# Optimization experiments

Hardware: AMD Instinct MI355X
Metric: run time of the kernel (lower is better)

The kernel has to match this reference:

```python
import jax, jax.numpy as jnp
import numpy as np

EXPERT_NUM = 8
SEQ_LEN = 2048
FREQ_LEN = SEQ_LEN // 2 + 1
B, C = 32, 512


def setup_inputs() -> dict:
    key = jax.random.key(0)
    k1, k2, k3 = jax.random.split(key, 3)
    x = jax.random.normal(k1, (B, C, SEQ_LEN), dtype=jnp.float32)
    band_boundaries = jax.random.uniform(k2, (EXPERT_NUM - 1,), dtype=jnp.float32)
    gate_w = jax.random.normal(k3, (EXPERT_NUM, FREQ_LEN), dtype=jnp.float32) / np.sqrt(FREQ_LEN)
    gate_b = jnp.zeros((EXPERT_NUM,), dtype=jnp.float32)
    return {"x": x, "band_boundaries": band_boundaries, "gate_w": gate_w, "gate_b": gate_b}


def reference(x, band_boundaries, gate_w, gate_b):
    # x: [B, C, L].  Normalize across channels per (batch, time) position.
    xp = jnp.transpose(x, (0, 2, 1))                       # [B, L, C]
    x_mean = jnp.mean(xp, axis=2, keepdims=True)           # [B, L, 1]
    xc = xp - x_mean
    x_var = jnp.var(xc, axis=2, keepdims=True, ddof=1) + 1e-5  # unbiased, as torch.var
    xn = xc / jnp.sqrt(x_var)
    x_norm = jnp.transpose(xn, (0, 2, 1))                  # [B, C, L]

    freq_x = jnp.fft.rfft(x_norm, axis=-1)                 # [B, C, F] complex
    F = FREQ_LEN

    # Learnable band boundaries -> integer bin boundaries per expert.
    b = jnp.sort(jax.nn.sigmoid(band_boundaries))
    b = jnp.concatenate([jnp.zeros((1,), b.dtype), b, jnp.ones((1,), b.dtype)])
    idx = (b * F).astype(jnp.int32)
    idx = idx.at[-1].set(F)                                # [E+1]

    # Per-frequency-bin expert membership: [E, F] 0/1 mask.
    f = jnp.arange(F)
    member = ((f[None, :] >= idx[:-1, None]) & (f[None, :] < idx[1:, None])).astype(x.dtype)

    # Gating over mean spectral magnitude.
    gating_input = jnp.abs(freq_x).mean(axis=1)            # [B, F]
    gating_scores = jax.nn.softmax(gating_input @ gate_w.T + gate_b, axis=-1)  # [B, E]

    # Fused: per-bin gate weight = sum_e g[b,e] * member[e,f] (no E copies of freq_x).
    w = gating_scores @ member                             # [B, F]
    combined_freq = freq_x * w[:, None, :].astype(freq_x.dtype)

    combined = jnp.fft.irfft(combined_freq, n=SEQ_LEN, axis=-1)  # [B, C, L]

    # De-normalize.
    cp = jnp.transpose(combined, (0, 2, 1))                # [B, L, C]
    out = cp * jnp.sqrt(x_var) + x_mean
    return jnp.transpose(out, (0, 2, 1))                   # [B, C, L]
```

## Files before the change

kernel.cpp:

```cpp
#include <hip/hip_runtime.h>
#include <math.h>

#define NB 32
#define NC 512
#define NF 1025

#define WS_MEAN 0
#define WS_SSTD 65536
#define WS_RSTD 131072
#define WS_GACC 196608
#define WS_WGT  229408
#define WS_PART 262208
#define WS_END_SPLIT (262208 + 262144)
#define WS_SPEC WS_END_SPLIT
#define WS_SPEC_FLOATS (NB * NC * 2048)
#define WS_END_CACHE (WS_SPEC + WS_SPEC_FLOATS)
#define WS_GPART WS_END_CACHE
#define WS_GPART_FLOATS (NB * 64 * NF)
#define WS_END_GPART (WS_GPART + WS_GPART_FLOATS)

#define PIDX(a) ((a) + ((a) >> 4))

__device__ __forceinline__ void lds_barrier() {
  __builtin_amdgcn_sched_barrier(0);
  asm volatile("s_waitcnt lgkmcnt(0)" ::: "memory");
  __builtin_amdgcn_s_barrier();
  __builtin_amdgcn_sched_barrier(0);
}

__device__ __forceinline__ void stage4_body(const float* __restrict__ sr,
                                            const float* __restrict__ si,
                                            float* __restrict__ dr,
                                            float* __restrict__ di,
                                            const int ls, const float w1c, const float w1s,
                                            const bool fwd) {
  const int t = threadIdx.x;
  const int s = 1 << ls;
  const int q = t & (s - 1);
  const int p = t >> ls;
  const float ar = sr[PIDX(t)],       ai = si[PIDX(t)];
  const float br = sr[PIDX(t + 256)], bi = si[PIDX(t + 256)];
  const float cr = sr[PIDX(t + 512)], ci = si[PIDX(t + 512)];
  const float er = sr[PIDX(t + 768)], ei = si[PIDX(t + 768)];
  const float apcr = ar + cr, apci = ai + ci;
  const float amcr = ar - cr, amci = ai - ci;
  const float bpdr = br + er, bpdi = bi + ei;
  const float bmdr = br - er, bmdi = bi - ei;
  const float w2r = w1c * w1c - w1s * w1s, w2i = 2.0f * w1c * w1s;
  const float w3r = w2r * w1c - w2i * w1s, w3i = w2r * w1s + w2i * w1c;
  float u1r, u1i, u3r, u3i;
  if (fwd) {
    u1r = amcr + bmdi; u1i = amci - bmdr;
    u3r = amcr - bmdi; u3i = amci + bmdr;
  } else {
    u1r = amcr - bmdi; u1i = amci + bmdr;
    u3r = amcr + bmdi; u3i = amci - bmdr;
  }
  const float x0r = apcr + bpdr, x0i = apci + bpdi;
  const float v2r = apcr - bpdr, v2i = apci - bpdi;
  const float x1r = w1c * u1r - w1s * u1i, x1i = w1c * u1i + w1s * u1r;
  const float x2r = w2r * v2r - w2i * v2i, x2i = w2r * v2i + w2i * v2r;
  const float x3r = w3r * u3r - w3i * u3i, x3i = w3r * u3i + w3i * u3r;
  const int base = q + ((p << 2) << ls);
  dr[PIDX(base)] = x0r;             di[PIDX(base)] = x0i;
  dr[PIDX(base + s)] = x1r;         di[PIDX(base + s)] = x1i;
  dr[PIDX(base + 2 * s)] = x2r;     di[PIDX(base + 2 * s)] = x2i;
  dr[PIDX(base + 3 * s)] = x3r;     di[PIDX(base + 3 * s)] = x3i;
}

__device__ __forceinline__ void stage4(const float* __restrict__ sr,
                                       const float* __restrict__ si,
                                       float* __restrict__ dr,
                                       float* __restrict__ di,
                                       const int ls, const float w1c, const float w1s,
                                       const bool fwd) {
  lds_barrier();
  stage4_body(sr, si, dr, di, ls, w1c, w1s, fwd);
}

__device__ __forceinline__ void stage0_reg(const float2 z0, const float2 z1,
                                           const float2 z2, const float2 z3,
                                           float* __restrict__ dr, float* __restrict__ di,
                                           const float w1c, const float w1s,
                                           const bool fwd) {
  const int t = threadIdx.x;
  const float apcr = z0.x + z2.x, apci = z0.y + z2.y;
  const float amcr = z0.x - z2.x, amci = z0.y - z2.y;
  const float bpdr = z1.x + z3.x, bpdi = z1.y + z3.y;
  const float bmdr = z1.x - z3.x, bmdi = z1.y - z3.y;
  const float w2r = w1c * w1c - w1s * w1s, w2i = 2.0f * w1c * w1s;
  const float w3r = w2r * w1c - w2i * w1s, w3i = w2r * w1s + w2i * w1c;
  float u1r, u1i, u3r, u3i;
  if (fwd) {
    u1r = amcr + bmdi; u1i = amci - bmdr;
    u3r = amcr - bmdi; u3i = amci + bmdr;
  } else {
    u1r = amcr - bmdi; u1i = amci + bmdr;
    u3r = amcr + bmdi; u3i = amci - bmdr;
  }
  const float x0r = apcr + bpdr, x0i = apci + bpdi;
  const float v2r = apcr - bpdr, v2i = apci - bpdi;
  const float x1r = w1c * u1r - w1s * u1i, x1i = w1c * u1i + w1s * u1r;
  const float x2r = w2r * v2r - w2i * v2i, x2i = w2r * v2i + w2i * v2r;
  const float x3r = w3r * u3r - w3i * u3i, x3i = w3r * u3i + w3i * u3r;
  const int base = t << 2;
  dr[PIDX(base)] = x0r;         di[PIDX(base)] = x0i;
  dr[PIDX(base + 1)] = x1r;     di[PIDX(base + 1)] = x1i;
  dr[PIDX(base + 2)] = x2r;     di[PIDX(base + 2)] = x2i;
  dr[PIDX(base + 3)] = x3r;     di[PIDX(base + 3)] = x3i;
}

__device__ __forceinline__ void stage_nt_body(const float* __restrict__ sr,
                                              const float* __restrict__ si,
                                              float2& o0, float2& o1, float2& o2, float2& o3,
                                              const bool fwd) {
  const int t = threadIdx.x;
  const float ar = sr[PIDX(t)],       ai = si[PIDX(t)];
  const float br = sr[PIDX(t + 256)], bi = si[PIDX(t + 256)];
  const float cr = sr[PIDX(t + 512)], ci = si[PIDX(t + 512)];
  const float er = sr[PIDX(t + 768)], ei = si[PIDX(t + 768)];
  const float apcr = ar + cr, apci = ai + ci;
  const float amcr = ar - cr, amci = ai - ci;
  const float bpdr = br + er, bpdi = bi + ei;
  const float bmdr = br - er, bmdi = bi - ei;
  float u1r, u1i, u3r, u3i;
  if (fwd) {
    u1r = amcr + bmdi; u1i = amci - bmdr;
    u3r = amcr - bmdi; u3i = amci + bmdr;
  } else {
    u1r = amcr - bmdi; u1i = amci + bmdr;
    u3r = amcr + bmdi; u3i = amci - bmdr;
  }
  o0.x = apcr + bpdr;  o0.y = apci + bpdi;
  o1.x = u1r;          o1.y = u1i;
  o2.x = apcr - bpdr;  o2.y = apci - bpdi;
  o3.x = u3r;          o3.y = u3i;
}

__device__ __forceinline__ void stage_nt_reg(const float* __restrict__ sr,
                                             const float* __restrict__ si,
                                             float2& o0, float2& o1, float2& o2, float2& o3,
                                             const bool fwd) {
  lds_barrier();
  stage_nt_body(sr, si, o0, o1, o2, o3, fwd);
}

__device__ __forceinline__ void fft_twiddles(int t, float& c0, float& s0,
                                             float& c1, float& s1,
                                             float& c2, float& s2,
                                             float& c3, float& s3) {
  __sincosf(-0.00613592315f * (float)t, &s0, &c0);
  __sincosf(-0.02454369261f * (float)(t >> 2), &s1, &c1);
  __sincosf(-0.09817477042f * (float)(t >> 4), &s2, &c2);
  __sincosf(-0.39269908170f * (float)(t >> 6), &s3, &c3);
}

__global__ __launch_bounds__(256) void kmoments(const float* __restrict__ x,
                                                float* __restrict__ ws) {
  const int b = blockIdx.x >> 3;
  const int l = ((blockIdx.x & 7) << 8) + threadIdx.x;
  const float* px = x + (size_t)b * (NC * 2048) + l;
  float sum = 0.f, sq = 0.f;
#pragma unroll 16
  for (int c = 0; c < NC; ++c) {
    float v = px[(size_t)c * 2048];
    sum += v;
    sq = fmaf(v, v, sq);
  }
  float mean = sum * (1.0f / 512.0f);
  float var = fmaf(-512.0f * mean, mean, sq) * (1.0f / 511.0f) + 1e-5f;
  float ss = sqrtf(var);
  int o = (b << 11) + l;
  ws[WS_MEAN + o] = mean;
  ws[WS_SSTD + o] = ss;
  ws[WS_RSTD + o] = 1.0f / ss;
}

__global__ __launch_bounds__(256) void kmoments_part(const float* __restrict__ x,
                                                     float* __restrict__ ws) {
  const int b = blockIdx.x >> 3;
  const int l = ((blockIdx.x & 7) << 8) + threadIdx.x;
  const int half = blockIdx.y;
  const float* px = x + (size_t)b * (NC * 2048) + (size_t)(half * 256) * 2048 + l;
  float sum = 0.f, sq = 0.f;
#pragma unroll 16
  for (int c = 0; c < 256; ++c) {
    float v = px[(size_t)c * 2048];
    sum += v;
    sq = fmaf(v, v, sq);
  }
  int o = (b << 11) + l;
  float2* part = (float2*)(ws + WS_PART) + (half << 16) + o;
  float2 pv; pv.x = sum; pv.y = sq;
  *part = pv;
}

__global__ __launch_bounds__(256) void kmoments_fin(float* __restrict__ ws) {
  const int o = blockIdx.x * 256 + threadIdx.x;
  const float2* part = (const float2*)(ws + WS_PART);
  float2 p0 = part[o];
  float2 p1 = part[(1 << 16) + o];
  float sum = p0.x + p1.x, sq = p0.y + p1.y;
  float mean = sum * (1.0f / 512.0f);
  float var = fmaf(-512.0f * mean, mean, sq) * (1.0f / 511.0f) + 1e-5f;
  float ss = sqrtf(var);
  ws[WS_MEAN + o] = mean;
  ws[WS_SSTD + o] = ss;
  ws[WS_RSTD + o] = 1.0f / ss;
}

__global__ __launch_bounds__(256) void kspec(const float* __restrict__ x,
                                             float* __restrict__ ws,
                                             float2* __restrict__ zout,
                                             float* __restrict__ gpart) {
  __shared__ float Ar[1088], Ai[1088], Br[1088], Bi[1088];
  const int tid = threadIdx.x;
  const int b = blockIdx.x >> 6;
  const int c0 = (blockIdx.x & 63) << 3;
  const float2* mean2 = (const float2*)(ws + WS_MEAN) + ((size_t)b << 10);
  const float2* rstd2 = (const float2*)(ws + WS_RSTD) + ((size_t)b << 10);
  float2 mv[4], rv[4];
#pragma unroll
  for (int j = 0; j < 4; ++j) {
    mv[j] = mean2[tid + (j << 8)];
    rv[j] = rstd2[tid + (j << 8)];
  }
  float w1s, w1c, w2s, w2c;
  __sincosf(-0.00306796158f * (float)tid, &w1s, &w1c);
  __sincosf(-0.00306796158f * (float)(tid + 256), &w2s, &w2c);
  float c0t, s0t, c1t, s1t, c2t, s2t, c3t, s3t;
  fft_twiddles(tid, c0t, s0t, c1t, s1t, c2t, s2t, c3t, s3t);
  float acc0 = 0.f, acc1 = 0.f, acc2 = 0.f, acc3 = 0.f, acc4 = 0.f;
  const float2* xrow = (const float2*)x + ((size_t)(b * NC + c0) << 10);
  float2 v[4];
#pragma unroll
  for (int j = 0; j < 4; ++j) v[j] = xrow[tid + (j << 8)];
  for (int r = 0; r < 8; ++r) {
    float2 zz[4];
#pragma unroll
    for (int j = 0; j < 4; ++j) {
      zz[j].x = (v[j].x - mv[j].x) * rv[j].x;
      zz[j].y = (v[j].y - mv[j].y) * rv[j].y;
    }
    if (r < 7) {
      const float2* nx = xrow + ((size_t)(r + 1) << 10);
#pragma unroll
      for (int j = 0; j < 4; ++j) v[j] = nx[tid + (j << 8)];
    }
    lds_barrier();
    stage0_reg(zz[0], zz[1], zz[2], zz[3], Br, Bi, c0t, s0t, true);
    stage4(Br, Bi, Ar, Ai, 2, c1t, s1t, true);
    stage4(Ar, Ai, Br, Bi, 4, c2t, s2t, true);
    stage4(Br, Bi, Ar, Ai, 6, c3t, s3t, true);
    float2 o0, o1, o2, o3;
    stage_nt_reg(Ar, Ai, o0, o1, o2, o3, true);
    Br[PIDX(tid)] = o0.x;        Bi[PIDX(tid)] = o0.y;
    Br[PIDX(tid + 256)] = o1.x;  Bi[PIDX(tid + 256)] = o1.y;
    Br[PIDX(tid + 512)] = o2.x;  Bi[PIDX(tid + 512)] = o2.y;
    Br[PIDX(tid + 768)] = o3.x;  Bi[PIDX(tid + 768)] = o3.y;
    lds_barrier();
    if (zout) {
      float2* zrow = zout + ((size_t)(b * NC + c0 + r) << 10);
      zrow[tid] = o0;
      zrow[tid + 256] = o1;
      zrow[tid + 512] = o2;
      zrow[tid + 768] = o3;
    }
    if (tid == 0) {
      float zr = Br[PIDX(0)], zi = Bi[PIDX(0)];
      acc0 += fabsf(zr + zi);
      acc1 += fabsf(zr - zi);
      float mr = Br[PIDX(512)], mi = Bi[PIDX(512)];
      acc4 += sqrtf(mr * mr + mi * mi);
    } else {
      const int k = tid;
      float zkr = Br[PIDX(k)], zki = Bi[PIDX(k)];
      float zmr = Br[PIDX(1024 - k)], zmi = Bi[PIDX(1024 - k)];
      float Ar_ = 0.5f * (zkr + zmr), Ai_ = 0.5f * (zki - zmi);
      float Br_ = 0.5f * (zki + zmi), Bi_ = -0.5f * (zkr - zmr);
      float WBr = Br_ * w1c - Bi_ * w1s, WBi = Br_ * w1s + Bi_ * w1c;
      float Xr = Ar_ + WBr, Xi = Ai_ + WBi;
      float Yr = Ar_ - WBr, Yi = Ai_ - WBi;
      acc0 += sqrtf(Xr * Xr + Xi * Xi);
      acc1 += sqrtf(Yr * Yr + Yi * Yi);
    }
    {
      const int k = tid + 256;
      float zkr = Br[PIDX(k)], zki = Bi[PIDX(k)];
      float zmr = Br[PIDX(1024 - k)], zmi = Bi[PIDX(1024 - k)];
      float Ar_ = 0.5f * (zkr + zmr), Ai_ = 0.5f * (zki - zmi);
      float Br_ = 0.5f * (zki + zmi), Bi_ = -0.5f * (zkr - zmr);
      float WBr = Br_ * w2c - Bi_ * w2s, WBi = Br_ * w2s + Bi_ * w2c;
      float Xr = Ar_ + WBr, Xi = Ai_ + WBi;
      float Yr = Ar_ - WBr, Yi = Ai_ - WBi;
      acc2 += sqrtf(Xr * Xr + Xi * Xi);
      acc3 += sqrtf(Yr * Yr + Yi * Yi);
    }
  }
  if (gpart) {
    float* prow = gpart + (size_t)blockIdx.x * NF;
    prow[tid] = acc0;
    prow[1024 - tid] = acc1;
    prow[tid + 256] = acc2;
    prow[768 - tid] = acc3;
    if (tid == 0) prow[512] = acc4;
  } else {
    float* g = ws + WS_GACC + b * NF;
    atomicAdd(g + tid, acc0);
    atomicAdd(g + 1024 - tid, acc1);
    atomicAdd(g + tid + 256, acc2);
    atomicAdd(g + 768 - tid, acc3);
    if (tid == 0) atomicAdd(g + 512, acc4);
  }
}

__global__ __launch_bounds__(256) void kgate(float* __restrict__ ws,
                                             const float* __restrict__ gw,
                                             const float* __restrict__ gb,
                                             const float* __restrict__ bb,
                                             const float* __restrict__ gpart) {
  const float* gacc = ws + WS_GACC;
  float* wgt = ws + WS_WGT;
  const int b = blockIdx.x;
  const int tid = threadIdx.x;
  __shared__ float red[256];
  __shared__ float sc[8];
  __shared__ int sidx[9];
  float acc[8];
#pragma unroll
  for (int e = 0; e < 8; ++e) acc[e] = 0.f;
  for (int f = tid; f < NF; f += 256) {
    float g;
    if (gpart) {
      const float* gp = gpart + (size_t)b * 64 * NF + f;
      g = 0.f;
#pragma unroll 8
      for (int j = 0; j < 64; ++j) g += gp[j * NF];
    } else {
      g = gacc[b * NF + f];
    }
    g *= (1.0f / 512.0f);
#pragma unroll
    for (int e = 0; e < 8; ++e) acc[e] = fmaf(g, gw[e * NF + f], acc[e]);
  }
#pragma unroll
  for (int e = 0; e < 8; ++e) {
    __syncthreads();
    red[tid] = acc[e];
    __syncthreads();
    for (int s2 = 128; s2 > 0; s2 >>= 1) {
      if (tid < s2) red[tid] += red[tid + s2];
      __syncthreads();
    }
    if (tid == 0) sc[e] = red[0] + gb[e];
  }
  __syncthreads();
  if (tid == 0) {
    float mx = sc[0];
    for (int e = 1; e < 8; ++e) mx = fmaxf(mx, sc[e]);
    float sum = 0.f;
    float ex[8];
    for (int e = 0; e < 8; ++e) { ex[e] = expf(sc[e] - mx); sum += ex[e]; }
    for (int e = 0; e < 8; ++e) sc[e] = ex[e] / sum;
    float sv[7];
    for (int i2 = 0; i2 < 7; ++i2) sv[i2] = 1.0f / (1.0f + expf(-bb[i2]));
    for (int i2 = 1; i2 < 7; ++i2) {
      float key = sv[i2];
      int j2 = i2 - 1;
      while (j2 >= 0 && sv[j2] > key) { sv[j2 + 1] = sv[j2]; --j2; }
      sv[j2 + 1] = key;
    }
    sidx[0] = 0;
    for (int i2 = 0; i2 < 7; ++i2) sidx[i2 + 1] = (int)(sv[i2] * 1025.0f);
    sidx[8] = 1025;
  }
  __syncthreads();
  for (int f = tid; f < NF; f += 256) {
    float wv = 0.f;
#pragma unroll
    for (int e = 0; e < 8; ++e)
      if (f >= sidx[e] && f < sidx[e + 1]) wv += sc[e];
    wgt[b * NF + f] = wv;
  }
}

__device__ __forceinline__ void combine_pair(float* __restrict__ zr_, float* __restrict__ zi_,
                                             int k, float wc, float ws_, float wk, float wmk) {
  const int ik = PIDX(k), im = PIDX(1024 - k);
  float zkr = zr_[ik], zki = zi_[ik];
  float zmr = zr_[im], zmi = zi_[im];
  float Ar_ = 0.5f * (zkr + zmr), Ai_ = 0.5f * (zki - zmi);
  float Br2 = 0.5f * (zki + zmi), Bi2 = -0.5f * (zkr - zmr);
  float WBr = Br2 * wc - Bi2 * ws_, WBi = Br2 * ws_ + Bi2 * wc;
  float Xr = Ar_ + WBr, Xi = Ai_ + WBi;
  float Xcr = Ar_ - WBr, Xci = Ai_ - WBi;
  float XpR = wk * Xr, XpI = wk * Xi;
  float XcpR = wmk * Xcr, XcpI = wmk * Xci;
  float Apr = 0.5f * (XpR + XcpR), Api = 0.5f * (XpI + XcpI);
  float Er = 0.5f * (XpR - XcpR), Ei = 0.5f * (XpI - XcpI);
  float Bpr = Er * wc + Ei * ws_;
  float Bpi = Ei * wc - Er * ws_;
  zr_[ik] = Apr - Bpi;  zi_[ik] = Api + Bpr;
  zr_[im] = Apr + Bpi;  zi_[im] = Bpr - Api;
}

__device__ __forceinline__ void combine_all(float* __restrict__ Br_, float* __restrict__ Bi_,
                                            const int tid,
                                            const float w1c, const float w1s,
                                            const float w2c, const float w2s,
                                            const float wk1, const float wm1,
                                            const float wk2, const float wm2,
                                            const float wmid) {
  if (tid == 0) {
    float zr = Br_[PIDX(0)], zi = Bi_[PIDX(0)];
    float X0 = (zr + zi) * wk1;
    float XM = (zr - zi) * wm1;
    Br_[PIDX(0)] = 0.5f * (X0 + XM);
    Bi_[PIDX(0)] = 0.5f * (X0 - XM);
    Br_[PIDX(512)] *= wmid;
    Bi_[PIDX(512)] *= wmid;
  } else {
    combine_pair(Br_, Bi_, tid, w1c, w1s, wk1, wm1);
  }
  combine_pair(Br_, Bi_, tid + 256, w2c, w2s, wk2, wm2);
}

__global__ __launch_bounds__(256) void kapply(const float* __restrict__ x,
                                              float* __restrict__ out,
                                              const float* __restrict__ ws) {
  __shared__ float Ar[1088], Ai[1088], Br[1088], Bi[1088];
  const int tid = threadIdx.x;
  const int b = blockIdx.x >> 9;
  const float2* mean2 = (const float2*)(ws + WS_MEAN) + ((size_t)b << 10);
  const float2* sstd2 = (const float2*)(ws + WS_SSTD) + ((size_t)b << 10);
  const float2* rstd2 = (const float2*)(ws + WS_RSTD) + ((size_t)b << 10);
  const float2* x2 = (const float2*)x + ((size_t)blockIdx.x << 10);
  const float* wrow = ws + WS_WGT + b * NF;
  float wk1 = wrow[tid];
  float wm1 = wrow[1024 - tid];
  float wk2 = wrow[tid + 256];
  float wm2 = wrow[768 - tid];
  float wmid = wrow[512];
  float w1s, w1c, w2s, w2c;
  __sincosf(-0.00306796158f * (float)tid, &w1s, &w1c);
  __sincosf(-0.00306796158f * (float)(tid + 256), &w2s, &w2c);
  float c0t, s0t, c1t, s1t, c2t, s2t, c3t, s3t;
  fft_twiddles(tid, c0t, s0t, c1t, s1t, c2t, s2t, c3t, s3t);
  float2 mv[4], rv[4], ssv[4];
#pragma unroll
  for (int j = 0; j < 4; ++j) {
    mv[j] = mean2[tid + (j << 8)];
    rv[j] = rstd2[tid + (j << 8)];
    ssv[j] = sstd2[tid + (j << 8)];
  }
  float2 zz[4];
#pragma unroll
  for (int j = 0; j < 4; ++j) {
    float2 v = x2[tid + (j << 8)];
    zz[j].x = (v.x - mv[j].x) * rv[j].x;
    zz[j].y = (v.y - mv[j].y) * rv[j].y;
  }
  stage0_reg(zz[0], zz[1], zz[2], zz[3], Br, Bi, c0t, s0t, true);
  stage4(Br, Bi, Ar, Ai, 2, c1t, s1t, true);
  stage4(Ar, Ai, Br, Bi, 4, c2t, s2t, true);
  stage4(Br, Bi, Ar, Ai, 6, c3t, s3t, true);
  float2 f0, f1, f2, f3;
  stage_nt_reg(Ar, Ai, f0, f1, f2, f3, true);
  Br[PIDX(tid)] = f0.x;        Bi[PIDX(tid)] = f0.y;
  Br[PIDX(tid + 256)] = f1.x;  Bi[PIDX(tid + 256)] = f1.y;
  Br[PIDX(tid + 512)] = f2.x;  Bi[PIDX(tid + 512)] = f2.y;
  Br[PIDX(tid + 768)] = f3.x;  Bi[PIDX(tid + 768)] = f3.y;
  lds_barrier();
  combine_all(Br, Bi, tid, w1c, w1s, w2c, w2s, wk1, wm1, wk2, wm2, wmid);
  stage4(Br, Bi, Ar, Ai, 0, c0t, -s0t, false);
  stage4(Ar, Ai, Br, Bi, 2, c1t, -s1t, false);
  stage4(Br, Bi, Ar, Ai, 4, c2t, -s2t, false);
  stage4(Ar, Ai, Br, Bi, 6, c3t, -s3t, false);
  float2 o0, o1, o2, o3;
  stage_nt_reg(Br, Bi, o0, o1, o2, o3, false);
  const float inv = 1.0f / 1024.0f;
  float2* out2 = (float2*)out + ((size_t)blockIdx.x << 10);
  float2 oo;
  oo.x = fmaf(o0.x * inv, ssv[0].x, mv[0].x);
  oo.y = fmaf(o0.y * inv, ssv[0].y, mv[0].y);
  out2[tid] = oo;
  oo.x = fmaf(o1.x * inv, ssv[1].x, mv[1].x);
  oo.y = fmaf(o1.y * inv, ssv[1].y, mv[1].y);
  out2[tid + 256] = oo;
  oo.x = fmaf(o2.x * inv, ssv[2].x, mv[2].x);
  oo.y = fmaf(o2.y * inv, ssv[2].y, mv[2].y);
  out2[tid + 512] = oo;
  oo.x = fmaf(o3.x * inv, ssv[3].x, mv[3].x);
  oo.y = fmaf(o3.y * inv, ssv[3].y, mv[3].y);
  out2[tid + 768] = oo;
}

__global__ __launch_bounds__(256) void kapply_z(const float2* __restrict__ z,
                                                float* __restrict__ out,
                                                const float* __restrict__ ws) {
  __shared__ float Ar[1088], Ai[1088], Br[1088], Bi[1088];
  const int tid = threadIdx.x;
  const int b = blockIdx.x >> 9;
  const float2* mean2 = (const float2*)(ws + WS_MEAN) + ((size_t)b << 10);
  const float2* sstd2 = (const float2*)(ws + WS_SSTD) + ((size_t)b << 10);
  const float* wrow = ws + WS_WGT + b * NF;
  float wk1 = wrow[tid];
  float wm1 = wrow[1024 - tid];
  float wk2 = wrow[tid + 256];
  float wm2 = wrow[768 - tid];
  float wmid = wrow[512];
  float w1s, w1c, w2s, w2c;
  __sincosf(-0.00306796158f * (float)tid, &w1s, &w1c);
  __sincosf(-0.00306796158f * (float)(tid + 256), &w2s, &w2c);
  float c0t, s0t, c1t, s1t, c2t, s2t, c3t, s3t;
  fft_twiddles(tid, c0t, s0t, c1t, s1t, c2t, s2t, c3t, s3t);
  const float2* zrow = z + ((size_t)blockIdx.x << 10);
  float2 mv[4], ssv[4];
#pragma unroll
  for (int j = 0; j < 4; ++j) {
    mv[j] = mean2[tid + (j << 8)];
    ssv[j] = sstd2[tid + (j << 8)];
  }
#pragma unroll
  for (int j = 0; j < 4; ++j) {
    const int n = tid + (j << 8);
    float2 v = zrow[n];
    Br[PIDX(n)] = v.x;
    Bi[PIDX(n)] = v.y;
  }
  lds_barrier();
  combine_all(Br, Bi, tid, w1c, w1s, w2c, w2s, wk1, wm1, wk2, wm2, wmid);
  stage4(Br, Bi, Ar, Ai, 0, c0t, -s0t, false);
  stage4(Ar, Ai, Br, Bi, 2, c1t, -s1t, false);
  stage4(Br, Bi, Ar, Ai, 4, c2t, -s2t, false);
  stage4(Ar, Ai, Br, Bi, 6, c3t, -s3t, false);
  float2 o0, o1, o2, o3;
  stage_nt_reg(Br, Bi, o0, o1, o2, o3, false);
  const float inv = 1.0f / 1024.0f;
  float2* out2 = (float2*)out + ((size_t)blockIdx.x << 10);
  float2 oo;
  oo.x = fmaf(o0.x * inv, ssv[0].x, mv[0].x);
  oo.y = fmaf(o0.y * inv, ssv[0].y, mv[0].y);
  out2[tid] = oo;
  oo.x = fmaf(o1.x * inv, ssv[1].x, mv[1].x);
  oo.y = fmaf(o1.y * inv, ssv[1].y, mv[1].y);
  out2[tid + 256] = oo;
  oo.x = fmaf(o2.x * inv, ssv[2].x, mv[2].x);
  oo.y = fmaf(o2.y * inv, ssv[2].y, mv[2].y);
  out2[tid + 512] = oo;
  oo.x = fmaf(o3.x * inv, ssv[3].x, mv[3].x);
  oo.y = fmaf(o3.y * inv, ssv[3].y, mv[3].y);
  out2[tid + 768] = oo;
}

extern "C" void kernel_launch(void* const* d_in, const int* in_sizes, int n_in,
                              void* d_out, int out_size, void* d_ws, size_t ws_size,
                              hipStream_t stream) {
  const float* x = (const float*)d_in[0];
  const float* bb = (const float*)d_in[1];
  const float* gw = (const float*)d_in[2];
  const float* gb = (const float*)d_in[3];
  float* ws = (float*)d_ws;
  float* out = (float*)d_out;

  const bool split = ws_size >= (size_t)WS_END_SPLIT * sizeof(float);
  const bool cache = ws_size >= (size_t)WS_END_CACHE * sizeof(float);
  const bool part = ws_size >= (size_t)WS_END_GPART * sizeof(float);

  if (!part) {
    hipMemsetAsync((char*)d_ws + WS_GACC * sizeof(float), 0, (NB * NF) * sizeof(float), stream);
  }
  if (split) {
    kmoments_part<<<dim3(NB * 8, 2), dim3(256), 0, stream>>>(x, ws);
    kmoments_fin<<<dim3(256), dim3(256), 0, stream>>>(ws);
  } else {
    kmoments<<<dim3(NB * 8), dim3(256), 0, stream>>>(x, ws);
  }
  kspec<<<dim3(NB * 64), dim3(256), 0, stream>>>(x, ws,
      cache ? (float2*)(ws + WS_SPEC) : nullptr,
      part ? (ws + WS_GPART) : nullptr);
  kgate<<<dim3(NB), dim3(256), 0, stream>>>(ws, gw, gb, bb,
      part ? (ws + WS_GPART) : nullptr);
  if (cache) {
    kapply_z<<<dim3(NB * NC), dim3(256), 0, stream>>>((const float2*)(ws + WS_SPEC), out, ws);
  } else {
    kapply<<<dim3(NB * NC), dim3(256), 0, stream>>>(x, out, ws);
  }
}
```

Before: 352.2 us.

## Interleave FFT shared buffers as float2 and precompute twiddle powers

Changes the LDS FFT scratch from separate real and imaginary float arrays to interleaved float2 arrays with a new padding scheme. Each element then moves in one 64-bit LDS access instead of two 32-bit ones, and stage0 writes use float4. Twiddle squares and cubes are now computed once per kernel rather than in every stage. The gating kernel also stops writing a full per-bin weight row. It stores only the expert scores and band indices, and the apply kernels rebuild per-bin weights in registers, which adds some ALU work and register pressure.

```diff
diff --git a/kernel.cpp b/kernel.cpp
--- a/kernel.cpp
+++ b/kernel.cpp
@@ -19,7 +19,7 @@
 #define WS_GPART_FLOATS (NB * 64 * NF)
 #define WS_END_GPART (WS_GPART + WS_GPART_FLOATS)
 
-#define PIDX(a) ((a) + ((a) >> 4))
+#define P2(a) ((a) + 2 * ((a) >> 4))
 
 __device__ __forceinline__ void lds_barrier() {
   __builtin_amdgcn_sched_barrier(0);
@@ -28,26 +28,31 @@
   __builtin_amdgcn_sched_barrier(0);
 }
 
-__device__ __forceinline__ void stage4_body(const float* __restrict__ sr,
-                                            const float* __restrict__ si,
-                                            float* __restrict__ dr,
-                                            float* __restrict__ di,
-                                            const int ls, const float w1c, const float w1s,
-                                            const bool fwd) {
+struct Tw { float c1, s1, c2, s2, c3, s3; };
+__device__ __forceinline__ Tw make_tw(float c, float s) {
+  Tw t;
+  t.c1 = c; t.s1 = s;
+  t.c2 = c * c - s * s;      t.s2 = 2.0f * c * s;
+  t.c3 = t.c2 * c - t.s2 * s; t.s3 = t.c2 * s + t.s2 * c;
+  return t;
+}
+__device__ __forceinline__ Tw conj_tw(Tw t) { t.s1 = -t.s1; t.s2 = -t.s2; t.s3 = -t.s3; return t; }
+
+__device__ __forceinline__ void stage4_body(const float2* __restrict__ src,
+                                            float2* __restrict__ dst,
+                                            const int ls, const Tw tw, const bool fwd) {
   const int t = threadIdx.x;
   const int s = 1 << ls;
   const int q = t & (s - 1);
   const int p = t >> ls;
-  const float ar = sr[PIDX(t)],       ai = si[PIDX(t)];
-  const float br = sr[PIDX(t + 256)], bi = si[PIDX(t + 256)];
-  const float cr = sr[PIDX(t + 512)], ci = si[PIDX(t + 512)];
-  const float er = sr[PIDX(t + 768)], ei = si[PIDX(t + 768)];
-  const float apcr = ar + cr, apci = ai + ci;
-  const float amcr = ar - cr, amci = ai - ci;
-  const float bpdr = br + er, bpdi = bi + ei;
-  const float bmdr = br - er, bmdi = bi - ei;
-  const float w2r = w1c * w1c - w1s * w1s, w2i = 2.0f * w1c * w1s;
-  const float w3r = w2r * w1c - w2i * w1s, w3i = w2r * w1s + w2i * w1c;
+  const float2 a = src[P2(t)];
+  const float2 b = src[P2(t + 256)];
+  const float2 c = src[P2(t + 512)];
+  const float2 e = src[P2(t + 768)];
+  const float apcr = a.x + c.x, apci = a.y + c.y;
+  const float amcr = a.x - c.x, amci = a.y - c.y;
+  const float bpdr = b.x + e.x, bpdi = b.y + e.y;
+  const float bmdr = b.x - e.x, bmdi = b.y - e.y;
   float u1r, u1i, u3r, u3i;
   if (fwd) {
     u1r = amcr + bmdi; u1i = amci - bmdr;
@@ -56,40 +61,30 @@
     u1r = amcr - bmdi; u1i = amci + bmdr;
     u3r = amcr + bmdi; u3i = amci - bmdr;
   }
-  const float x0r = apcr + bpdr, x0i = apci + bpdi;
   const float v2r = apcr - bpdr, v2i = apci - bpdi;
-  const float x1r = w1c * u1r - w1s * u1i, x1i = w1c * u1i + w1s * u1r;
-  const float x2r = w2r * v2r - w2i * v2i, x2i = w2r * v2i + w2i * v2r;
-  const float x3r = w3r * u3r - w3i * u3i, x3i = w3r * u3i + w3i * u3r;
   const int base = q + ((p << 2) << ls);
-  dr[PIDX(base)] = x0r;             di[PIDX(base)] = x0i;
-  dr[PIDX(base + s)] = x1r;         di[PIDX(base + s)] = x1i;
-  dr[PIDX(base + 2 * s)] = x2r;     di[PIDX(base + 2 * s)] = x2i;
-  dr[PIDX(base + 3 * s)] = x3r;     di[PIDX(base + 3 * s)] = x3i;
-}
-
-__device__ __forceinline__ void stage4(const float* __restrict__ sr,
-                                       const float* __restrict__ si,
-                                       float* __restrict__ dr,
-                                       float* __restrict__ di,
-                                       const int ls, const float w1c, const float w1s,
-                                       const bool fwd) {
+  dst[P2(base)] = make_float2(apcr + bpdr, apci + bpdi);
+  dst[P2(base + s)] = make_float2(tw.c1 * u1r - tw.s1 * u1i, tw.c1 * u1i + tw.s1 * u1r);
+  dst[P2(base + 2 * s)] = make_float2(tw.c2 * v2r - tw.s2 * v2i, tw.c2 * v2i + tw.s2 * v2r);
+  dst[P2(base + 3 * s)] = make_float2(tw.c3 * u3r - tw.s3 * u3i, tw.c3 * u3i + tw.s3 * u3r);
+}
+
+__device__ __forceinline__ void stage4(const float2* __restrict__ src,
+                                       float2* __restrict__ dst,
+                                       const int ls, const Tw tw, const bool fwd) {
   lds_barrier();
-  stage4_body(sr, si, dr, di, ls, w1c, w1s, fwd);
+  stage4_body(src, dst, ls, tw, fwd);
 }
 
 __device__ __forceinline__ void stage0_reg(const float2 z0, const float2 z1,
                                            const float2 z2, const float2 z3,
-                                           float* __restrict__ dr, float* __restrict__ di,
-                                           const float w1c, const float w1s,
-                                           const bool fwd) {
+                                           float2* __restrict__ dst,
+                                           const Tw tw, const bool fwd) {
   const int t = threadIdx.x;
   const float apcr = z0.x + z2.x, apci = z0.y + z2.y;
   const float amcr = z0.x - z2.x, amci = z0.y - z2.y;
   const float bpdr = z1.x + z3.x, bpdi = z1.y + z3.y;
   const float bmdr = z1.x - z3.x, bmdi = z1.y - z3.y;
-  const float w2r = w1c * w1c - w1s * w1s, w2i = 2.0f * w1c * w1s;
-  const float w3r = w2r * w1c - w2i * w1s, w3i = w2r * w1s + w2i * w1c;
   float u1r, u1i, u3r, u3i;
   if (fwd) {
     u1r = amcr + bmdi; u1i = amci - bmdr;
@@ -98,31 +93,26 @@
     u1r = amcr - bmdi; u1i = amci + bmdr;
     u3r = amcr + bmdi; u3i = amci - bmdr;
   }
-  const float x0r = apcr + bpdr, x0i = apci + bpdi;
   const float v2r = apcr - bpdr, v2i = apci - bpdi;
-  const float x1r = w1c * u1r - w1s * u1i, x1i = w1c * u1i + w1s * u1r;
-  const float x2r = w2r * v2r - w2i * v2i, x2i = w2r * v2i + w2i * v2r;
-  const float x3r = w3r * u3r - w3i * u3i, x3i = w3r * u3i + w3i * u3r;
-  const int base = t << 2;
-  dr[PIDX(base)] = x0r;         di[PIDX(base)] = x0i;
-  dr[PIDX(base + 1)] = x1r;     di[PIDX(base + 1)] = x1i;
-  dr[PIDX(base + 2)] = x2r;     di[PIDX(base + 2)] = x2i;
-  dr[PIDX(base + 3)] = x3r;     di[PIDX(base + 3)] = x3i;
-}
-
-__device__ __forceinline__ void stage_nt_body(const float* __restrict__ sr,
-                                              const float* __restrict__ si,
+  float4* d4 = (float4*)&dst[P2(t << 2)];
+  d4[0] = make_float4(apcr + bpdr, apci + bpdi,
+                      tw.c1 * u1r - tw.s1 * u1i, tw.c1 * u1i + tw.s1 * u1r);
+  d4[1] = make_float4(tw.c2 * v2r - tw.s2 * v2i, tw.c2 * v2i + tw.s2 * v2r,
+                      tw.c3 * u3r - tw.s3 * u3i, tw.c3 * u3i + tw.s3 * u3r);
+}
+
+__device__ __forceinline__ void stage_nt_body(const float2* __restrict__ src,
                                               float2& o0, float2& o1, float2& o2, float2& o3,
                                               const bool fwd) {
   const int t = threadIdx.x;
-  const float ar = sr[PIDX(t)],       ai = si[PIDX(t)];
-  const float br = sr[PIDX(t + 256)], bi = si[PIDX(t + 256)];
-  const float cr = sr[PIDX(t + 512)], ci = si[PIDX(t + 512)];
-  const float er = sr[PIDX(t + 768)], ei = si[PIDX(t + 768)];
-  const float apcr = ar + cr, apci = ai + ci;
-  const float amcr = ar - cr, amci = ai - ci;
-  const float bpdr = br + er, bpdi = bi + ei;
-  const float bmdr = br - er, bmdi = bi - ei;
+  const float2 a = src[P2(t)];
+  const float2 b = src[P2(t + 256)];
+  const float2 c = src[P2(t + 512)];
+  const float2 e = src[P2(t + 768)];
+  const float apcr = a.x + c.x, apci = a.y + c.y;
+  const float amcr = a.x - c.x, amci = a.y - c.y;
+  const float bpdr = b.x + e.x, bpdi = b.y + e.y;
+  const float bmdr = b.x - e.x, bmdi = b.y - e.y;
   float u1r, u1i, u3r, u3i;
   if (fwd) {
     u1r = amcr + bmdi; u1i = amci - bmdr;
@@ -131,28 +121,25 @@
     u1r = amcr - bmdi; u1i = amci + bmdr;
     u3r = amcr + bmdi; u3i = amci - bmdr;
   }
-  o0.x = apcr + bpdr;  o0.y = apci + bpdi;
-  o1.x = u1r;          o1.y = u1i;
-  o2.x = apcr - bpdr;  o2.y = apci - bpdi;
-  o3.x = u3r;          o3.y = u3i;
-}
-
-__device__ __forceinline__ void stage_nt_reg(const float* __restrict__ sr,
-                                             const float* __restrict__ si,
+  o0 = make_float2(apcr + bpdr, apci + bpdi);
+  o1 = make_float2(u1r, u1i);
+  o2 = make_float2(apcr - bpdr, apci - bpdi);
+  o3 = make_float2(u3r, u3i);
+}
+
+__device__ __forceinline__ void stage_nt_reg(const float2* __restrict__ src,
                                              float2& o0, float2& o1, float2& o2, float2& o3,
                                              const bool fwd) {
   lds_barrier();
-  stage_nt_body(sr, si, o0, o1, o2, o3, fwd);
-}
-
-__device__ __forceinline__ void fft_twiddles(int t, float& c0, float& s0,
-                                             float& c1, float& s1,
-                                             float& c2, float& s2,
-                                             float& c3, float& s3) {
-  __sincosf(-0.00613592315f * (float)t, &s0, &c0);
-  __sincosf(-0.02454369261f * (float)(t >> 2), &s1, &c1);
-  __sincosf(-0.09817477042f * (float)(t >> 4), &s2, &c2);
-  __sincosf(-0.39269908170f * (float)(t >> 6), &s3, &c3);
+  stage_nt_body(src, o0, o1, o2, o3, fwd);
+}
+
+__device__ __forceinline__ void fft_tws(int t, Tw& t0, Tw& t1, Tw& t2, Tw& t3) {
+  float c, s;
+  __sincosf(-0.00613592315f * (float)t, &s, &c);        t0 = make_tw(c, s);
+  __sincosf(-0.02454369261f * (float)(t >> 2), &s, &c); t1 = make_tw(c, s);
+  __sincosf(-0.09817477042f * (float)(t >> 4), &s, &c); t2 = make_tw(c, s);
+  __sincosf(-0.39269908170f * (float)(t >> 6), &s, &c); t3 = make_tw(c, s);
 }
 
 __global__ __launch_bounds__(256) void kmoments(const float* __restrict__ x,
@@ -213,7 +200,7 @@
                                              float* __restrict__ ws,
                                              float2* __restrict__ zout,
                                              float* __restrict__ gpart) {
-  __shared__ float Ar[1088], Ai[1088], Br[1088], Bi[1088];
+  __shared__ __align__(16) float2 A[1152], B[1152];
   const int tid = threadIdx.x;
   const int b = blockIdx.x >> 6;
   const int c0 = (blockIdx.x & 63) << 3;
@@ -228,8 +215,8 @@
   float w1s, w1c, w2s, w2c;
   __sincosf(-0.00306796158f * (float)tid, &w1s, &w1c);
   __sincosf(-0.00306796158f * (float)(tid + 256), &w2s, &w2c);
-  float c0t, s0t, c1t, s1t, c2t, s2t, c3t, s3t;
-  fft_twiddles(tid, c0t, s0t, c1t, s1t, c2t, s2t, c3t, s3t);
+  Tw t0, t1, t2, t3;
+  fft_tws(tid, t0, t1, t2, t3);
   float acc0 = 0.f, acc1 = 0.f, acc2 = 0.f, acc3 = 0.f, acc4 = 0.f;
   const float2* xrow = (const float2*)x + ((size_t)(b * NC + c0) << 10);
   float2 v[4];
@@ -248,16 +235,16 @@
       for (int j = 0; j < 4; ++j) v[j] = nx[tid + (j << 8)];
     }
     lds_barrier();
-    stage0_reg(zz[0], zz[1], zz[2], zz[3], Br, Bi, c0t, s0t, true);
-    stage4(Br, Bi, Ar, Ai, 2, c1t, s1t, true);
-    stage4(Ar, Ai, Br, Bi, 4, c2t, s2t, true);
-    stage4(Br, Bi, Ar, Ai, 6, c3t, s3t, true);
+    stage0_reg(zz[0], zz[1], zz[2], zz[3], B, t0, true);
+    stage4(B, A, 2, t1, true);
+    stage4(A, B, 4, t2, true);
+    stage4(B, A, 6, t3, true);
     float2 o0, o1, o2, o3;
-    stage_nt_reg(Ar, Ai, o0, o1, o2, o3, true);
-    Br[PIDX(tid)] = o0.x;        Bi[PIDX(tid)] = o0.y;
-    Br[PIDX(tid + 256)] = o1.x;  Bi[PIDX(tid + 256)] = o1.y;
-    Br[PIDX(tid + 512)] = o2.x;  Bi[PIDX(tid + 512)] = o2.y;
-    Br[PIDX(tid + 768)] = o3.x;  Bi[PIDX(tid + 768)] = o3.y;
+    stage_nt_reg(A, o0, o1, o2, o3, true);
+    B[P2(tid)] = o0;
+    B[P2(tid + 256)] = o1;
+    B[P2(tid + 512)] = o2;
+    B[P2(tid + 768)] = o3;
     lds_barrier();
     if (zout) {
       float2* zrow = zout + ((size_t)(b * NC + c0 + r) << 10);
@@ -267,18 +254,17 @@
       zrow[tid + 768] = o3;
     }
     if (tid == 0) {
-      float zr = Br[PIDX(0)], zi = Bi[PIDX(0)];
-      acc0 += fabsf(zr + zi);
-      acc1 += fabsf(zr - zi);
-      float mr = Br[PIDX(512)], mi = Bi[PIDX(512)];
-      acc4 += sqrtf(mr * mr + mi * mi);
+      float2 z0 = B[P2(0)];
+      acc0 += fabsf(z0.x + z0.y);
+      acc1 += fabsf(z0.x - z0.y);
+      float2 zm = B[P2(512)];
+      acc4 += sqrtf(zm.x * zm.x + zm.y * zm.y);
     } else {
       const int k = tid;
-      float zkr = Br[PIDX(k)], zki = Bi[PIDX(k)];
-      float zmr = Br[PIDX(1024 - k)], zmi = Bi[PIDX(1024 - k)];
-      float Ar_ = 0.5f * (zkr + zmr), Ai_ = 0.5f * (zki - zmi);
-      float Br_ = 0.5f * (zki + zmi), Bi_ = -0.5f * (zkr - zmr);
-      float WBr = Br_ * w1c - Bi_ * w1s, WBi = Br_ * w1s + Bi_ * w1c;
+      float2 zk = B[P2(k)], zm = B[P2(1024 - k)];
+      float Ar_ = 0.5f * (zk.x + zm.x), Ai_ = 0.5f * (zk.y - zm.y);
+      float Bq = 0.5f * (zk.y + zm.y), Bi2 = -0.5f * (zk.x - zm.x);
+      float WBr = Bq * w1c - Bi2 * w1s, WBi = Bq * w1s + Bi2 * w1c;
       float Xr = Ar_ + WBr, Xi = Ai_ + WBi;
       float Yr = Ar_ - WBr, Yi = Ai_ - WBi;
       acc0 += sqrtf(Xr * Xr + Xi * Xi);
@@ -286,11 +272,10 @@
     }
     {
       const int k = tid + 256;
-      float zkr = Br[PIDX(k)], zki = Bi[PIDX(k)];
-      float zmr = Br[PIDX(1024 - k)], zmi = Bi[PIDX(1024 - k)];
-      float Ar_ = 0.5f * (zkr + zmr), Ai_ = 0.5f * (zki - zmi);
-      float Br_ = 0.5f * (zki + zmi), Bi_ = -0.5f * (zkr - zmr);
-      float WBr = Br_ * w2c - Bi_ * w2s, WBi = Br_ * w2s + Bi_ * w2c;
+      float2 zk = B[P2(k)], zm = B[P2(1024 - k)];
+      float Ar_ = 0.5f * (zk.x + zm.x), Ai_ = 0.5f * (zk.y - zm.y);
+      float Bq = 0.5f * (zk.y + zm.y), Bi2 = -0.5f * (zk.x - zm.x);
+      float WBr = Bq * w2c - Bi2 * w2s, WBi = Bq * w2s + Bi2 * w2c;
       float Xr = Ar_ + WBr, Xi = Ai_ + WBi;
       float Yr = Ar_ - WBr, Yi = Ai_ - WBi;
       acc2 += sqrtf(Xr * Xr + Xi * Xi);
@@ -320,12 +305,9 @@
                                              const float* __restrict__ bb,
                                              const float* __restrict__ gpart) {
   const float* gacc = ws + WS_GACC;
-  float* wgt = ws + WS_WGT;
   const int b = blockIdx.x;
   const int tid = threadIdx.x;
   __shared__ float red[256];
-  __shared__ float sc[8];
-  __shared__ int sidx[9];
   float acc[8];
 #pragma unroll
   for (int e = 0; e < 8; ++e) acc[e] = 0.f;
@@ -343,6 +325,7 @@
 #pragma unroll
     for (int e = 0; e < 8; ++e) acc[e] = fmaf(g, gw[e * NF + f], acc[e]);
   }
+  float sc[8];
 #pragma unroll
   for (int e = 0; e < 8; ++e) {
     __syncthreads();
@@ -354,7 +337,6 @@
     }
     if (tid == 0) sc[e] = red[0] + gb[e];
   }
-  __syncthreads();
   if (tid == 0) {
     float mx = sc[0];
     for (int e = 1; e < 8; ++e) mx = fmaxf(mx, sc[e]);
@@ -370,27 +352,20 @@
       while (j2 >= 0 && sv[j2] > key) { sv[j2 + 1] = sv[j2]; --j2; }
       sv[j2 + 1] = key;
     }
-    sidx[0] = 0;
-    for (int i2 = 0; i2 < 7; ++i2) sidx[i2 + 1] = (int)(sv[i2] * 1025.0f);
-    sidx[8] = 1025;
-  }
-  __syncthreads();
-  for (int f = tid; f < NF; f += 256) {
-    float wv = 0.f;
-#pragma unroll
-    for (int e = 0; e < 8; ++e)
-      if (f >= sidx[e] && f < sidx[e + 1]) wv += sc[e];
-    wgt[b * NF + f] = wv;
-  }
-}
-
-__device__ __forceinline__ void combine_pair(float* __restrict__ zr_, float* __restrict__ zi_,
+    float* srow = ws + WS_WGT + (b << 5);
+    for (int e = 0; e < 8; ++e) srow[e] = sc[e];
+    srow[8] = 0.0f;
+    for (int i2 = 0; i2 < 7; ++i2) srow[9 + i2] = (float)((int)(sv[i2] * 1025.0f));
+    srow[16] = 1025.0f;
+  }
+}
+
+__device__ __forceinline__ void combine_pair(float2* __restrict__ z,
                                              int k, float wc, float ws_, float wk, float wmk) {
-  const int ik = PIDX(k), im = PIDX(1024 - k);
-  float zkr = zr_[ik], zki = zi_[ik];
-  float zmr = zr_[im], zmi = zi_[im];
-  float Ar_ = 0.5f * (zkr + zmr), Ai_ = 0.5f * (zki - zmi);
-  float Br2 = 0.5f * (zki + zmi), Bi2 = -0.5f * (zkr - zmr);
+  const int ik = P2(k), im = P2(1024 - k);
+  float2 zk = z[ik], zm = z[im];
+  float Ar_ = 0.5f * (zk.x + zm.x), Ai_ = 0.5f * (zk.y - zm.y);
+  float Br2 = 0.5f * (zk.y + zm.y), Bi2 = -0.5f * (zk.x - zm.x);
   float WBr = Br2 * wc - Bi2 * ws_, WBi = Br2 * ws_ + Bi2 * wc;
   float Xr = Ar_ + WBr, Xi = Ai_ + WBi;
   float Xcr = Ar_ - WBr, Xci = Ai_ - WBi;
@@ -400,52 +375,63 @@
   float Er = 0.5f * (XpR - XcpR), Ei = 0.5f * (XpI - XcpI);
   float Bpr = Er * wc + Ei * ws_;
   float Bpi = Ei * wc - Er * ws_;
-  zr_[ik] = Apr - Bpi;  zi_[ik] = Api + Bpr;
-  zr_[im] = Apr + Bpi;  zi_[im] = Bpr - Api;
-}
-
-__device__ __forceinline__ void combine_all(float* __restrict__ Br_, float* __restrict__ Bi_,
-                                            const int tid,
+  z[ik] = make_float2(Apr - Bpi, Api + Bpr);
+  z[im] = make_float2(Apr + Bpi, Bpr - Api);
+}
+
+__device__ __forceinline__ void combine_all(float2* __restrict__ z, const int tid,
                                             const float w1c, const float w1s,
                                             const float w2c, const float w2s,
                                             const float wk1, const float wm1,
                                             const float wk2, const float wm2,
                                             const float wmid) {
   if (tid == 0) {
-    float zr = Br_[PIDX(0)], zi = Bi_[PIDX(0)];
-    float X0 = (zr + zi) * wk1;
-    float XM = (zr - zi) * wm1;
-    Br_[PIDX(0)] = 0.5f * (X0 + XM);
-    Bi_[PIDX(0)] = 0.5f * (X0 - XM);
-    Br_[PIDX(512)] *= wmid;
-    Bi_[PIDX(512)] *= wmid;
-  } else {
-    combine_pair(Br_, Bi_, tid, w1c, w1s, wk1, wm1);
-  }
-  combine_pair(Br_, Bi_, tid + 256, w2c, w2s, wk2, wm2);
-}
+    float2 z0 = z[P2(0)];
+    float X0 = (z0.x + z0.y) * wk1;
+    float XM = (z0.x - z0.y) * wm1;
+    z[P2(0)] = make_float2(0.5f * (X0 + XM), 0.5f * (X0 - XM));
+    float2 zm = z[P2(512)];
+    z[P2(512)] = make_float2(zm.x * wmid, zm.y * wmid);
+  } else {
+    combine_pair(z, tid, w1c, w1s, wk1, wm1);
+  }
+  combine_pair(z, tid + 256, w2c, w2s, wk2, wm2);
+}
+
+#define BANDW(ff, siv, scv, dst) { float wv = 0.f; \
+    _Pragma("unroll") \
+    for (int e = 0; e < 8; ++e) \
+      wv += ((ff) >= siv[e] && (ff) < siv[e + 1]) ? scv[e] : 0.f; \
+    dst = wv; }
 
 __global__ __launch_bounds__(256) void kapply(const float* __restrict__ x,
                                               float* __restrict__ out,
                                               const float* __restrict__ ws) {
-  __shared__ float Ar[1088], Ai[1088], Br[1088], Bi[1088];
+  __shared__ __align__(16) float2 A[1152], B[1152];
   const int tid = threadIdx.x;
   const int b = blockIdx.x >> 9;
   const float2* mean2 = (const float2*)(ws + WS_MEAN) + ((size_t)b << 10);
   const float2* sstd2 = (const float2*)(ws + WS_SSTD) + ((size_t)b << 10);
   const float2* rstd2 = (const float2*)(ws + WS_RSTD) + ((size_t)b << 10);
   const float2* x2 = (const float2*)x + ((size_t)blockIdx.x << 10);
-  const float* wrow = ws + WS_WGT + b * NF;
-  float wk1 = wrow[tid];
-  float wm1 = wrow[1024 - tid];
-  float wk2 = wrow[tid + 256];
-  float wm2 = wrow[768 - tid];
-  float wmid = wrow[512];
+  const float* srow = ws + WS_WGT + (b << 5);
+  float scv[8], siv[9];
+#pragma unroll
+  for (int e = 0; e < 8; ++e) scv[e] = srow[e];
+#pragma unroll
+  for (int e = 0; e < 9; ++e) siv[e] = srow[8 + e];
+  float wk1, wm1, wk2, wm2, wmid;
+  BANDW((float)tid, siv, scv, wk1);
+  BANDW((float)(1024 - tid), siv, scv, wm1);
+  BANDW((float)(tid + 256), siv, scv, wk2);
+  BANDW((float)(768 - tid), siv, scv, wm2);
+  BANDW(512.0f, siv, scv, wmid);
   float w1s, w1c, w2s, w2c;
   __sincosf(-0.00306796158f * (float)tid, &w1s, &w1c);
   __sincosf(-0.00306796158f * (float)(tid + 256), &w2s, &w2c);
-  float c0t, s0t, c1t, s1t, c2t, s2t, c3t, s3t;
-  fft_twiddles(tid, c0t, s0t, c1t, s1t, c2t, s2t, c3t, s3t);
+  Tw t0, t1, t2, t3;
+  fft_tws(tid, t0, t1, t2, t3);
+  const Tw i0 = conj_tw(t0), i1 = conj_tw(t1), i2 = conj_tw(t2), i3 = conj_tw(t3);
   float2 mv[4], rv[4], ssv[4];
 #pragma unroll
   for (int j = 0; j < 4; ++j) {
@@ -460,24 +446,24 @@
     zz[j].x = (v.x - mv[j].x) * rv[j].x;
     zz[j].y = (v.y - mv[j].y) * rv[j].y;
   }
-  stage0_reg(zz[0], zz[1], zz[2], zz[3], Br, Bi, c0t, s0t, true);
-  stage4(Br, Bi, Ar, Ai, 2, c1t, s1t, true);
-  stage4(Ar, Ai, Br, Bi, 4, c2t, s2t, true);
-  stage4(Br, Bi, Ar, Ai, 6, c3t, s3t, true);
+  stage0_reg(zz[0], zz[1], zz[2], zz[3], B, t0, true);
+  stage4(B, A, 2, t1, true);
+  stage4(A, B, 4, t2, true);
+  stage4(B, A, 6, t3, true);
   float2 f0, f1, f2, f3;
-  stage_nt_reg(Ar, Ai, f0, f1, f2, f3, true);
-  Br[PIDX(tid)] = f0.x;        Bi[PIDX(tid)] = f0.y;
-  Br[PIDX(tid + 256)] = f1.x;  Bi[PIDX(tid + 256)] = f1.y;
-  Br[PIDX(tid + 512)] = f2.x;  Bi[PIDX(tid + 512)] = f2.y;
-  Br[PIDX(tid + 768)] = f3.x;  Bi[PIDX(tid + 768)] = f3.y;
+  stage_nt_reg(A, f0, f1, f2, f3, true);
+  B[P2(tid)] = f0;
+  B[P2(tid + 256)] = f1;
+  B[P2(tid + 512)] = f2;
+  B[P2(tid + 768)] = f3;
   lds_barrier();
-  combine_all(Br, Bi, tid, w1c, w1s, w2c, w2s, wk1, wm1, wk2, wm2, wmid);
-  stage4(Br, Bi, Ar, Ai, 0, c0t, -s0t, false);
-  stage4(Ar, Ai, Br, Bi, 2, c1t, -s1t, false);
-  stage4(Br, Bi, Ar, Ai, 4, c2t, -s2t, false);
-  stage4(Ar, Ai, Br, Bi, 6, c3t, -s3t, false);
+  combine_all(B, tid, w1c, w1s, w2c, w2s, wk1, wm1, wk2, wm2, wmid);
+  stage4(B, A, 0, i0, false);
+  stage4(A, B, 2, i1, false);
+  stage4(B, A, 4, i2, false);
+  stage4(A, B, 6, i3, false);
   float2 o0, o1, o2, o3;
-  stage_nt_reg(Br, Bi, o0, o1, o2, o3, false);
+  stage_nt_reg(B, o0, o1, o2, o3, false);
   const float inv = 1.0f / 1024.0f;
   float2* out2 = (float2*)out + ((size_t)blockIdx.x << 10);
   float2 oo;
@@ -498,22 +484,29 @@
 __global__ __launch_bounds__(256) void kapply_z(const float2* __restrict__ z,
                                                 float* __restrict__ out,
                                                 const float* __restrict__ ws) {
-  __shared__ float Ar[1088], Ai[1088], Br[1088], Bi[1088];
+  __shared__ __align__(16) float2 A[1152], B[1152];
   const int tid = threadIdx.x;
   const int b = blockIdx.x >> 9;
   const float2* mean2 = (const float2*)(ws + WS_MEAN) + ((size_t)b << 10);
   const float2* sstd2 = (const float2*)(ws + WS_SSTD) + ((size_t)b << 10);
-  const float* wrow = ws + WS_WGT + b * NF;
-  float wk1 = wrow[tid];
-  float wm1 = wrow[1024 - tid];
-  float wk2 = wrow[tid + 256];
-  float wm2 = wrow[768 - tid];
-  float wmid = wrow[512];
+  const float* srow = ws + WS_WGT + (b << 5);
+  float scv[8], siv[9];
+#pragma unroll
+  for (int e = 0; e < 8; ++e) scv[e] = srow[e];
+#pragma unroll
+  for (int e = 0; e < 9; ++e) siv[e] = srow[8 + e];
+  float wk1, wm1, wk2, wm2, wmid;
+  BANDW((float)tid, siv, scv, wk1);
+  BANDW((float)(1024 - tid), siv, scv, wm1);
+  BANDW((float)(tid + 256), siv, scv, wk2);
+  BANDW((float)(768 - tid), siv, scv, wm2);
+  BANDW(512.0f, siv, scv, wmid);
   float w1s, w1c, w2s, w2c;
   __sincosf(-0.00306796158f * (float)tid, &w1s, &w1c);
   __sincosf(-0.00306796158f * (float)(tid + 256), &w2s, &w2c);
-  float c0t, s0t, c1t, s1t, c2t, s2t, c3t, s3t;
-  fft_twiddles(tid, c0t, s0t, c1t, s1t, c2t, s2t, c3t, s3t);
+  Tw t0, t1, t2, t3;
+  fft_tws(tid, t0, t1, t2, t3);
+  const Tw i0 = conj_tw(t0), i1 = conj_tw(t1), i2 = conj_tw(t2), i3 = conj_tw(t3);
   const float2* zrow = z + ((size_t)blockIdx.x << 10);
   float2 mv[4], ssv[4];
 #pragma unroll
@@ -524,18 +517,16 @@
 #pragma unroll
   for (int j = 0; j < 4; ++j) {
     const int n = tid + (j << 8);
-    float2 v = zrow[n];
-    Br[PIDX(n)] = v.x;
-    Bi[PIDX(n)] = v.y;
+    B[P2(n)] = zrow[n];
   }
   lds_barrier();
-  combine_all(Br, Bi, tid, w1c, w1s, w2c, w2s, wk1, wm1, wk2, wm2, wmid);
-  stage4(Br, Bi, Ar, Ai, 0, c0t, -s0t, false);
-  stage4(Ar, Ai, Br, Bi, 2, c1t, -s1t, false);
-  stage4(Br, Bi, Ar, Ai, 4, c2t, -s2t, false);
-  stage4(Ar, Ai, Br, Bi, 6, c3t, -s3t, false);
+  combine_all(B, tid, w1c, w1s, w2c, w2s, wk1, wm1, wk2, wm2, wmid);
+  stage4(B, A, 0, i0, false);
+  stage4(A, B, 2, i1, false);
+  stage4(B, A, 4, i2, false);
+  stage4(A, B, 6, i3, false);
   float2 o0, o1, o2, o3;
-  stage_nt_reg(Br, Bi, o0, o1, o2, o3, false);
+  stage_nt_reg(B, o0, o1, o2, o3, false);
   const float inv = 1.0f / 1024.0f;
   float2* out2 = (float2*)out + ((size_t)blockIdx.x << 10);
   float2 oo;
```

Measured after the change: 345.7 us. Within noise of the previous version (-1.9%).
